# Performance work log

Hardware: AMD Instinct MI355X
Metric: run time of the kernel (lower is better)

## Reference

```python
import jax, jax.numpy as jnp
import numpy as np

B, S, D = 4, 1024, 1024
H, G = 16, 8            # num_heads, num_query_groups
HD = D // H             # head_dim = 64
E, TOPK, ED = 8, 2, 2 * D   # experts, top_k, expert_dim
GH = D // 2             # gate hidden
EPS = 1e-5


def setup_inputs() -> dict:
    key = jax.random.key(0)
    ks = iter(jax.random.split(key, 32))
    rn = lambda shape, s=0.02: jax.random.normal(next(ks), shape, jnp.float32) * s
    return {
        "x": jax.random.normal(next(ks), (B, S, D), jnp.float32),
        # GQA projections (stored [in, out])
        "wq": rn((D, G * HD)), "bq": jnp.zeros((G * HD,), jnp.float32),
        "wk": rn((D, D)), "bk": jnp.zeros((D,), jnp.float32),
        "wv": rn((D, D)), "bv": jnp.zeros((D,), jnp.float32),
        "wo": rn((D, D)), "bo": jnp.zeros((D,), jnp.float32),
        # LayerNorms
        "ln1_g": jnp.ones((D,), jnp.float32), "ln1_b": jnp.zeros((D,), jnp.float32),
        "ln2_g": jnp.ones((D,), jnp.float32), "ln2_b": jnp.zeros((D,), jnp.float32),
        # MoE gate: Linear(D, D//2) -> ReLU -> Linear(D//2, E)
        "gw1": rn((D, GH)), "gb1": jnp.zeros((GH,), jnp.float32),
        "gw2": rn((GH, E)), "gb2": jnp.zeros((E,), jnp.float32),
        # stacked expert FFNs: Linear(D, ED) -> GELU -> Linear(ED, D)
        "ew1": rn((E, D, ED)), "eb1": jnp.zeros((E, ED), jnp.float32),
        "ew2": rn((E, ED, D)), "eb2": jnp.zeros((E, D), jnp.float32),
    }


def _layernorm(x, g, b):
    mu = jnp.mean(x, axis=-1, keepdims=True)
    var = jnp.var(x, axis=-1, keepdims=True)
    return (x - mu) * jax.lax.rsqrt(var + EPS) * g + b


def _block(x, wq, bq, wk, bk, wv, bv, wo, bo, ln1_g, ln1_b, ln2_g, ln2_b,
           gw1, gb1, gw2, gb2, ew1, eb1, ew2, eb2):
    # --- GQA self-attention (dropout is identity in eval) ---
    h = _layernorm(x, ln1_g, ln1_b)
    q = (h @ wq + bq).reshape(B, S, G, HD).transpose(0, 2, 1, 3)   # [B,G,S,hd]
    k = (h @ wk + bk).reshape(B, S, H, HD).transpose(0, 2, 1, 3)   # [B,H,S,hd]
    v = (h @ wv + bv).reshape(B, S, H, HD).transpose(0, 2, 1, 3)
    q = jnp.repeat(q, H // G, axis=1)                              # repeat_interleave -> [B,H,S,hd]
    scores = jnp.einsum("bhqd,bhkd->bhqk", q, k) * (HD ** -0.5)
    attn = jax.nn.softmax(scores, axis=-1)
    ao = jnp.einsum("bhqk,bhkd->bhqd", attn, v)
    ao = ao.transpose(0, 2, 1, 3).reshape(B, S, D) @ wo + bo
    x = x + ao

    # --- MoE FFN ---
    h2 = _layernorm(x, ln2_g, ln2_b).reshape(-1, D)                # [T,D], T=B*S
    gate_logits = jax.nn.relu(h2 @ gw1 + gb1) @ gw2 + gb2          # [T,E]
    gate_w = jax.nn.softmax(gate_logits, axis=-1)
    top_w, top_i = jax.lax.top_k(gate_w, TOPK)                     # [T,k]
    top_w = jax.nn.softmax(top_w, axis=-1)                         # renormalize among top-k
    combine = jnp.sum(jax.nn.one_hot(top_i, E, dtype=h2.dtype) * top_w[..., None], axis=1)  # [T,E]
    hid = jax.nn.gelu(jnp.einsum("td,edh->teh", h2, ew1) + eb1, approximate=False)          # [T,E,ED]
    expert_out = jnp.einsum("teh,ehd->ted", hid, ew2) + eb2        # [T,E,D]
    moe = jnp.einsum("ted,te->td", expert_out, combine).reshape(B, S, D)
    return x + moe


def reference(x, wq, bq, wk, bk, wv, bv, wo, bo, ln1_g, ln1_b, ln2_g, ln2_b,
              gw1, gb1, gw2, gb2, ew1, eb1, ew2, eb2):
    return _block(x, wq, bq, wk, bk, wv, bv, wo, bo, ln1_g, ln1_b, ln2_g, ln2_b,
                  gw1, gb1, gw2, gb2, ew1, eb1, ew2, eb2)
```

## Files before the change

kernel.cpp:

```cpp
#include <hip/hip_runtime.h>

typedef __bf16 bf16x8 __attribute__((ext_vector_type(8)));
typedef float f32x4 __attribute__((ext_vector_type(4)));
typedef unsigned int u32x4 __attribute__((ext_vector_type(4)));
typedef unsigned int u32x2 __attribute__((ext_vector_type(2)));

#define DEV static __device__ __forceinline__

DEV unsigned short f2bf(float f) {
  unsigned int u = __builtin_bit_cast(unsigned int, f);
  u += 0x7fffu + ((u >> 16) & 1u);
  return (unsigned short)(u >> 16);
}
DEV float bf2f(unsigned int hbits) { return __builtin_bit_cast(float, hbits << 16); }

DEV bf16x8 load_bf8(const unsigned short* p) {
  u32x4 u = *(const u32x4*)p;
  return __builtin_bit_cast(bf16x8, u);
}
DEV void unpack8(u32x4 u, float f[8]) {
  f[0] = bf2f(u.x & 0xffffu); f[1] = bf2f(u.x >> 16);
  f[2] = bf2f(u.y & 0xffffu); f[3] = bf2f(u.y >> 16);
  f[4] = bf2f(u.z & 0xffffu); f[5] = bf2f(u.z >> 16);
  f[6] = bf2f(u.w & 0xffffu); f[7] = bf2f(u.w >> 16);
}
DEV void gload_lds16(const void* g, void* l) {
  __builtin_amdgcn_global_load_lds((const __attribute__((address_space(1))) void*)g,
                                   (__attribute__((address_space(3))) void*)l, 16, 0, 0);
}
DEV f32x4 mfma16(bf16x8 a, bf16x8 b, f32x4 c) {
  return __builtin_amdgcn_mfma_f32_16x16x32_bf16(a, b, c, 0, 0, 0);
}

__global__ __launch_bounds__(256) void cm_transpose(
    const float* __restrict__ src, unsigned short* __restrict__ dst,
    int K, int N, long srcStrideE, long dstStrideE) {
  src += (long)blockIdx.z * srcStrideE;
  dst += (long)blockIdx.z * dstStrideE;
  __shared__ float t[32][33];
  const int n0 = blockIdx.x * 32, k0 = blockIdx.y * 32;
  const int tx = threadIdx.x & 31, ty = threadIdx.x >> 5;
#pragma unroll
  for (int j = 0; j < 4; ++j) {
    int k = k0 + ty + j * 8, n = n0 + tx;
    if (k < K && n < N) t[ty + j * 8][tx] = src[(long)k * N + n];
  }
  __syncthreads();
#pragma unroll
  for (int j = 0; j < 4; ++j) {
    int n = n0 + ty + j * 8, k = k0 + tx;
    if (n < N && k < K) dst[(long)n * K + k] = f2bf(t[tx][ty + j * 8]);
  }
}

__global__ __launch_bounds__(256) void cm_transpose_split(
    const float* __restrict__ src, unsigned short* __restrict__ dhi,
    unsigned short* __restrict__ dlo, int K, int N) {
  __shared__ float t[32][33];
  const int n0 = blockIdx.x * 32, k0 = blockIdx.y * 32;
  const int tx = threadIdx.x & 31, ty = threadIdx.x >> 5;
#pragma unroll
  for (int j = 0; j < 4; ++j) {
    int k = k0 + ty + j * 8, n = n0 + tx;
    if (k < K && n < N) t[ty + j * 8][tx] = src[(long)k * N + n];
  }
  __syncthreads();
#pragma unroll
  for (int j = 0; j < 4; ++j) {
    int n = n0 + ty + j * 8, k = k0 + tx;
    if (n < N && k < K) {
      float v = t[tx][ty + j * 8];
      unsigned short hi = f2bf(v);
      dhi[(long)n * K + k] = hi;
      dlo[(long)n * K + k] = f2bf(v - bf2f(hi));
    }
  }
}

template <bool WLO>
__global__ __launch_bounds__(256) void cm_ln(
    const float* __restrict__ x, const float* __restrict__ g, const float* __restrict__ b,
    unsigned short* __restrict__ ob, unsigned short* __restrict__ olo) {
  const int row = blockIdx.x, tid = threadIdx.x;
  const f32x4 v = *(const f32x4*)(x + (long)row * 1024 + tid * 4);
  float s1 = v[0] + v[1] + v[2] + v[3];
  float s2 = v[0] * v[0] + v[1] * v[1] + v[2] * v[2] + v[3] * v[3];
#pragma unroll
  for (int m = 32; m >= 1; m >>= 1) { s1 += __shfl_xor(s1, m); s2 += __shfl_xor(s2, m); }
  __shared__ float r1[4], r2[4];
  if ((tid & 63) == 0) { r1[tid >> 6] = s1; r2[tid >> 6] = s2; }
  __syncthreads();
  s1 = r1[0] + r1[1] + r1[2] + r1[3];
  s2 = r2[0] + r2[1] + r2[2] + r2[3];
  const float mean = s1 * (1.f / 1024.f);
  const float rs = rsqrtf(s2 * (1.f / 1024.f) - mean * mean + 1e-5f);
  const f32x4 gg = *(const f32x4*)(g + tid * 4);
  const f32x4 bb = *(const f32x4*)(b + tid * 4);
  float o[4];
  unsigned short hi[4];
#pragma unroll
  for (int i = 0; i < 4; ++i) {
    o[i] = (v[i] - mean) * rs * gg[i] + bb[i];
    hi[i] = f2bf(o[i]);
  }
  u32x2 pk;
  pk.x = (unsigned)hi[0] | ((unsigned)hi[1] << 16);
  pk.y = (unsigned)hi[2] | ((unsigned)hi[3] << 16);
  *(u32x2*)(ob + (long)row * 1024 + tid * 4) = pk;
  if (WLO) {
    u32x2 pl;
    pl.x = (unsigned)f2bf(o[0] - bf2f(hi[0])) | ((unsigned)f2bf(o[1] - bf2f(hi[1])) << 16);
    pl.y = (unsigned)f2bf(o[2] - bf2f(hi[2])) | ((unsigned)f2bf(o[3] - bf2f(hi[3])) << 16);
    *(u32x2*)(olo + (long)row * 1024 + tid * 4) = pl;
  }
}

enum { EP_BF16 = 0, EP_RELU = 1, EP_GELU = 2, EP_RES_F32 = 3 };

template <int EPI, int MODE>
__global__ __launch_bounds__(256, 2) void cm_gemm_bt(
    const unsigned short* __restrict__ A, int lda,
    const unsigned short* __restrict__ BT, long btStrideE, int ldb,
    const float* __restrict__ bias, int biasStrideE,
    const float* __restrict__ res,
    void* __restrict__ outp, int ldc,
    int M, int K,
    const int* __restrict__ cnt, const int* __restrict__ offs,
    const int* __restrict__ rowidx) {
  int bx, by, z;
  if (MODE == 0) {
    const int gx = gridDim.x, gy = gridDim.y;
    const int nwg = gx * gy;
    int flat = (int)blockIdx.x + gx * (int)blockIdx.y;
    const int q = nwg >> 3, r = nwg & 7, xcd = flat & 7, idx = flat >> 3;
    flat = (xcd < r ? xcd * (q + 1) : r * (q + 1) + (xcd - r) * q) + idx;
    bx = flat % gx; by = flat / gx; z = 0;
  } else {
    bx = blockIdx.x; by = blockIdx.y; z = blockIdx.z;
  }

  int valid = M, rowbase = 0;
  const unsigned short* Bp = BT;
  const float* biasp = bias;
  if (MODE > 0) {
    valid = cnt[z];
    if (by * 128 >= valid) return;
    rowbase = offs[z];
    Bp += (long)z * btStrideE;
    biasp += (long)z * biasStrideE;
  }
  const int tid = threadIdx.x;
  const int brow = by * 128, bcol = bx * 128;
  const int wid = tid >> 6, lane = tid & 63;
  const int wr = wid >> 1, wc = wid & 1;

  const int srow = tid >> 3, sc = tid & 7;
  const int scg = ((sc ^ (srow & 7)) << 3);
  const int ldst = srow * 64 + sc * 8;

  __shared__ __align__(16) unsigned short As[128 * 64];
  __shared__ __align__(16) unsigned short Bs[128 * 64];

  long asrc[4], bsrc[4];
#pragma unroll
  for (int i = 0; i < 4; ++i) {
    int m = brow + srow + i * 32;
    if (MODE == 0) {
      asrc[i] = (long)m * lda;
    } else {
      int p = m < valid ? m : valid - 1;
      if (MODE == 1) asrc[i] = (long)rowidx[z * 4096 + p] * lda;
      else           asrc[i] = (long)(rowbase + p) * lda;
    }
    bsrc[i] = (long)(bcol + srow + i * 32) * ldb;
  }

  f32x4 acc[4][4] = {};

  for (int k0 = 0; k0 < K; k0 += 64) {
#pragma unroll
    for (int i = 0; i < 4; ++i) {
      gload_lds16(A + asrc[i] + k0 + scg, &As[ldst + i * 2048]);
      gload_lds16(Bp + bsrc[i] + k0 + scg, &Bs[ldst + i * 2048]);
    }
    __syncthreads();
#pragma unroll
    for (int ks = 0; ks < 2; ++ks) {
      bf16x8 af[4], bfr[4];
#pragma unroll
      for (int m = 0; m < 4; ++m) {
        const int r = wr * 64 + m * 16 + (lane & 15);
        af[m] = load_bf8(&As[r * 64 + (((ks * 4 + (lane >> 4)) ^ (lane & 7)) << 3)]);
      }
#pragma unroll
      for (int n = 0; n < 4; ++n) {
        const int r = wc * 64 + n * 16 + (lane & 15);
        bfr[n] = load_bf8(&Bs[r * 64 + (((ks * 4 + (lane >> 4)) ^ (lane & 7)) << 3)]);
      }
#pragma unroll
      for (int m = 0; m < 4; ++m)
#pragma unroll
        for (int n = 0; n < 4; ++n)
          acc[m][n] = mfma16(af[m], bfr[n], acc[m][n]);
    }
    __syncthreads();
  }

#pragma unroll
  for (int m = 0; m < 4; ++m) {
#pragma unroll
    for (int rr = 0; rr < 4; ++rr) {
      const int lrow = brow + wr * 64 + m * 16 + (lane >> 4) * 4 + rr;
      if (MODE > 0 && lrow >= valid) continue;
      const long orow = (long)(rowbase + lrow);
#pragma unroll
      for (int n = 0; n < 4; ++n) {
        const int gcol = bcol + wc * 64 + n * 16 + (lane & 15);
        float vv = acc[m][n][rr] + biasp[gcol];
        if constexpr (EPI == EP_RELU) vv = fmaxf(vv, 0.f);
        if constexpr (EPI == EP_GELU) vv = 0.5f * vv * (1.f + erff(vv * 0.70710678f));
        if constexpr (EPI == EP_RES_F32)
          ((float*)outp)[orow * ldc + gcol] = vv + res[orow * ldc + gcol];
        else
          ((unsigned short*)outp)[orow * ldc + gcol] = f2bf(vv);
      }
    }
  }
}

__global__ __launch_bounds__(256, 2) void cm_gemm_gate(
    const unsigned short* __restrict__ Ah, const unsigned short* __restrict__ Al,
    const unsigned short* __restrict__ Bh, const unsigned short* __restrict__ Bl,
    const float* __restrict__ bias, float* __restrict__ C) {
  const int tid = threadIdx.x;
  const int brow = blockIdx.y * 128, bcol = blockIdx.x * 128;
  const int wid = tid >> 6, lane = tid & 63;
  const int wr = wid >> 1, wc = wid & 1;
  const int srow0 = tid >> 2, scol = (tid & 3) * 8;

  __shared__ __align__(16) unsigned short Ash[128 * 32], Asl[128 * 32];
  __shared__ __align__(16) unsigned short Bsh[128 * 32], Bsl[128 * 32];

  f32x4 acc[4][4] = {};

  for (int k0 = 0; k0 < 1024; k0 += 32) {
#pragma unroll
    for (int i = 0; i < 2; ++i) {
      const long ar = (long)(brow + srow0 + i * 64) * 1024 + k0 + scol;
      const long br = (long)(bcol + srow0 + i * 64) * 1024 + k0 + scol;
      const int lo = (srow0 + i * 64) * 32 + scol;
      gload_lds16(Ah + ar, &Ash[lo]);
      gload_lds16(Al + ar, &Asl[lo]);
      gload_lds16(Bh + br, &Bsh[lo]);
      gload_lds16(Bl + br, &Bsl[lo]);
    }
    __syncthreads();
    bf16x8 ah[4], al[4], bh[4], bl[4];
#pragma unroll
    for (int m = 0; m < 4; ++m) {
      const int ro = (wr * 64 + m * 16 + (lane & 15)) * 32 + (lane >> 4) * 8;
      ah[m] = load_bf8(&Ash[ro]); al[m] = load_bf8(&Asl[ro]);
    }
#pragma unroll
    for (int n = 0; n < 4; ++n) {
      const int ro = (wc * 64 + n * 16 + (lane & 15)) * 32 + (lane >> 4) * 8;
      bh[n] = load_bf8(&Bsh[ro]); bl[n] = load_bf8(&Bsl[ro]);
    }
#pragma unroll
    for (int m = 0; m < 4; ++m)
#pragma unroll
      for (int n = 0; n < 4; ++n) {
        acc[m][n] = mfma16(al[m], bh[n], acc[m][n]);
        acc[m][n] = mfma16(ah[m], bl[n], acc[m][n]);
        acc[m][n] = mfma16(ah[m], bh[n], acc[m][n]);
      }
    __syncthreads();
  }

#pragma unroll
  for (int m = 0; m < 4; ++m)
#pragma unroll
    for (int rr = 0; rr < 4; ++rr) {
      const long orow = brow + wr * 64 + m * 16 + (lane >> 4) * 4 + rr;
#pragma unroll
      for (int n = 0; n < 4; ++n) {
        const int gcol = bcol + wc * 64 + n * 16 + (lane & 15);
        C[orow * 512 + gcol] = fmaxf(acc[m][n][rr] + bias[gcol], 0.f);
      }
    }
}

__global__ __launch_bounds__(256) void cm_vtrans(
    const unsigned short* __restrict__ qkv, unsigned short* __restrict__ Vt) {
  const int stile = blockIdx.x, bh = blockIdx.y;
  const int b = bh >> 4, h = bh & 15;
  const int tid = threadIdx.x;
  __shared__ __align__(16) unsigned short t[64][72];
  const int d0 = (tid & 7) * 8, sl = tid >> 3;
#pragma unroll
  for (int i = 0; i < 2; ++i) {
    const int s = sl + i * 32;
    *(u32x4*)&t[s][d0] =
        *(const u32x4*)(qkv + (long)(b * 1024 + stile * 64 + s) * 2560 + 1536 + h * 64 + d0);
  }
  __syncthreads();
  const int s0 = (tid & 7) * 8, dl = tid >> 3;
#pragma unroll
  for (int i = 0; i < 2; ++i) {
    const int d = dl + i * 32;
    unsigned short vals[8];
#pragma unroll
    for (int j = 0; j < 8; ++j) vals[j] = t[s0 + j][d];
    u32x4 u;
    u.x = vals[0] | ((unsigned)vals[1] << 16);
    u.y = vals[2] | ((unsigned)vals[3] << 16);
    u.z = vals[4] | ((unsigned)vals[5] << 16);
    u.w = vals[6] | ((unsigned)vals[7] << 16);
    *(u32x4*)(Vt + (long)(bh * 64 + d) * 1024 + stile * 64 + s0) = u;
  }
}

__global__ __launch_bounds__(256, 2) void cm_attn(
    const unsigned short* __restrict__ qkv,
    const unsigned short* __restrict__ Vt,
    unsigned short* __restrict__ ao) {
  const int qt = blockIdx.x, bh = blockIdx.y;
  const int b = bh >> 4, h = bh & 15, g = h >> 1;
  const int tid = threadIdx.x, wid = tid >> 6, lane = tid & 63;
  const int q0 = qt * 32;

  __shared__ __align__(16) unsigned short sc[32][1032];
  __shared__ float rowrcp[32];

  bf16x8 bq[2][2];
#pragma unroll
  for (int nf = 0; nf < 2; ++nf)
#pragma unroll
    for (int ks = 0; ks < 2; ++ks)
      bq[nf][ks] = load_bf8(qkv + (long)(b * 1024 + q0 + nf * 16 + (lane & 15)) * 2560 +
                            g * 64 + ks * 32 + (lane >> 4) * 8);

#pragma unroll 1
  for (int c = 0; c < 4; ++c) {
    const int kb = wid * 256 + c * 64;
    f32x4 acc[4][2] = {};
#pragma unroll
    for (int ks = 0; ks < 2; ++ks) {
      bf16x8 ak[4];
#pragma unroll
      for (int mf = 0; mf < 4; ++mf)
        ak[mf] = load_bf8(qkv + (long)(b * 1024 + kb + mf * 16 + (lane & 15)) * 2560 +
                          512 + h * 64 + ks * 32 + (lane >> 4) * 8);
#pragma unroll
      for (int mf = 0; mf < 4; ++mf)
#pragma unroll
        for (int nf = 0; nf < 2; ++nf)
          acc[mf][nf] = mfma16(ak[mf], bq[nf][ks], acc[mf][nf]);
    }
#pragma unroll
    for (int mf = 0; mf < 4; ++mf)
#pragma unroll
      for (int nf = 0; nf < 2; ++nf) {
        const int q = nf * 16 + (lane & 15);
        const int key = kb + mf * 16 + (lane >> 4) * 4;
        u32x2 pk;
        pk.x = (unsigned)f2bf(acc[mf][nf][0] * 0.125f) |
               ((unsigned)f2bf(acc[mf][nf][1] * 0.125f) << 16);
        pk.y = (unsigned)f2bf(acc[mf][nf][2] * 0.125f) |
               ((unsigned)f2bf(acc[mf][nf][3] * 0.125f) << 16);
        *(u32x2*)&sc[q][key] = pk;
      }
  }
  __syncthreads();

  {
    const int row = tid >> 3, seg = tid & 7;
    float mx = -1e30f;
#pragma unroll
    for (int i = 0; i < 16; ++i) {
      float f[8];
      unpack8(*(const u32x4*)&sc[row][i * 64 + seg * 8], f);
#pragma unroll
      for (int j = 0; j < 8; ++j) mx = fmaxf(mx, f[j]);
    }
#pragma unroll
    for (int m = 4; m >= 1; m >>= 1) mx = fmaxf(mx, __shfl_xor(mx, m));
    float sum = 0.f;
#pragma unroll 1
    for (int i = 0; i < 16; ++i) {
      float f[8];
      unpack8(*(const u32x4*)&sc[row][i * 64 + seg * 8], f);
      float e[8];
#pragma unroll
      for (int j = 0; j < 8; ++j) { e[j] = __expf(f[j] - mx); sum += e[j]; }
      u32x4 o;
      o.x = (unsigned)f2bf(e[0]) | ((unsigned)f2bf(e[1]) << 16);
      o.y = (unsigned)f2bf(e[2]) | ((unsigned)f2bf(e[3]) << 16);
      o.z = (unsigned)f2bf(e[4]) | ((unsigned)f2bf(e[5]) << 16);
      o.w = (unsigned)f2bf(e[6]) | ((unsigned)f2bf(e[7]) << 16);
      *(u32x4*)&sc[row][i * 64 + seg * 8] = o;
    }
#pragma unroll
    for (int m = 4; m >= 1; m >>= 1) sum += __shfl_xor(sum, m);
    if (seg == 0) rowrcp[row] = 1.f / sum;
  }
  __syncthreads();

  {
    f32x4 acc[2] = {};
    const unsigned short* vtb = Vt + (long)bh * 64 * 1024;
#pragma unroll 4
    for (int k0 = 0; k0 < 1024; k0 += 32) {
      const bf16x8 bv =
          load_bf8(vtb + (long)(wid * 16 + (lane & 15)) * 1024 + k0 + (lane >> 4) * 8);
#pragma unroll
      for (int m = 0; m < 2; ++m) {
        const bf16x8 ap = load_bf8(&sc[m * 16 + (lane & 15)][k0 + (lane >> 4) * 8]);
        acc[m] = mfma16(ap, bv, acc[m]);
      }
    }
#pragma unroll
    for (int m = 0; m < 2; ++m)
#pragma unroll
      for (int rr = 0; rr < 4; ++rr) {
        const int q = m * 16 + (lane >> 4) * 4 + rr;
        const int d = wid * 16 + (lane & 15);
        ao[(long)(b * 1024 + q0 + q) * 1024 + h * 64 + d] = f2bf(acc[m][rr] * rowrcp[q]);
      }
  }
}

__global__ __launch_bounds__(64) void cm_route_pick(
    const float* __restrict__ g1f, const float* __restrict__ gw2, const float* __restrict__ gb2,
    int* __restrict__ pick, int* __restrict__ slot_e, float* __restrict__ rwt) {
  const int t = blockIdx.x, lane = threadIdx.x;
  f32x4 a0 = *(const f32x4*)(g1f + (long)t * 512 + lane * 8);
  f32x4 a1 = *(const f32x4*)(g1f + (long)t * 512 + lane * 8 + 4);
  float logit[8];
#pragma unroll
  for (int e = 0; e < 8; ++e) {
    float s = 0.f;
#pragma unroll
    for (int j = 0; j < 4; ++j) {
      s += a0[j] * gw2[(lane * 8 + j) * 8 + e];
      s += a1[j] * gw2[(lane * 8 + 4 + j) * 8 + e];
    }
#pragma unroll
    for (int m = 32; m >= 1; m >>= 1) s += __shfl_xor(s, m);
    logit[e] = s + gb2[e];
  }
  float mx = logit[0];
#pragma unroll
  for (int e = 1; e < 8; ++e) mx = fmaxf(mx, logit[e]);
  float p[8], sum = 0.f;
#pragma unroll
  for (int e = 0; e < 8; ++e) { p[e] = __expf(logit[e] - mx); sum += p[e]; }
  const float rs = 1.f / sum;
#pragma unroll
  for (int e = 0; e < 8; ++e) p[e] *= rs;
  int i0 = 0;
#pragma unroll
  for (int e = 1; e < 8; ++e) if (p[e] > p[i0]) i0 = e;
  int i1 = (i0 == 0) ? 1 : 0;
#pragma unroll
  for (int e = 0; e < 8; ++e) if (e != i0 && p[e] > p[i1]) i1 = e;
  const float w0 = 1.f / (1.f + __expf(p[i1] - p[i0]));
  if (lane == 0) {
    pick[t] = i0 | (i1 << 8);
    slot_e[t * 2] = i0; slot_e[t * 2 + 1] = i1;
    rwt[t * 2] = w0;    rwt[t * 2 + 1] = 1.f - w0;
  }
}

__global__ __launch_bounds__(256) void cm_route_place(
    const int* __restrict__ pick, int* __restrict__ cnt,
    int* __restrict__ etok, int* __restrict__ slot_p) {
  const int t = blockIdx.x * 256 + threadIdx.x;
  const int lane = threadIdx.x & 63;
  const int pk = pick[t];
  const int p0 = pk & 15, p1 = (pk >> 8) & 15;
  const unsigned long long lt = ((unsigned long long)1 << lane) - 1;
  int my_r0 = 0, my_c0p1 = 0, my_r1 = 0, tot = 0;
#pragma unroll
  for (int e = 0; e < 8; ++e) {
    const unsigned long long m0 = __ballot(p0 == e);
    const unsigned long long m1 = __ballot(p1 == e);
    if (p0 == e) my_r0 = __popcll(m0 & lt);
    if (p1 == e) { my_c0p1 = __popcll(m0); my_r1 = __popcll(m1 & lt); }
    if (lane == e) tot = __popcll(m0) + __popcll(m1);
  }
  int base = 0;
  if (lane < 8 && tot > 0) base = atomicAdd(&cnt[lane], tot);
  const int b0 = __shfl(base, p0);
  const int b1 = __shfl(base, p1);
  const int pos0 = b0 + my_r0;
  const int pos1 = b1 + my_c0p1 + my_r1;
  etok[p0 * 4096 + pos0] = t;
  etok[p1 * 4096 + pos1] = t;
  slot_p[t * 2] = pos0;
  slot_p[t * 2 + 1] = pos1;
}

__global__ void cm_offs(const int* __restrict__ cnt, int* __restrict__ offs) {
  if (threadIdx.x == 0) {
    int s = 0;
#pragma unroll
    for (int e = 0; e < 8; ++e) { offs[e] = s; s += cnt[e]; }
  }
}

__global__ __launch_bounds__(256) void cm_combine(
    const float* __restrict__ x2, const unsigned short* __restrict__ eo,
    const int* __restrict__ slot_e, const int* __restrict__ slot_p,
    const float* __restrict__ rwt, const int* __restrict__ offs,
    float* __restrict__ outp) {
  const int t = blockIdx.x, tid = threadIdx.x;
  const long r0 = (long)(offs[slot_e[t * 2]] + slot_p[t * 2]);
  const long r1 = (long)(offs[slot_e[t * 2 + 1]] + slot_p[t * 2 + 1]);
  const float w0 = rwt[t * 2], w1 = rwt[t * 2 + 1];
  const f32x4 xv = *(const f32x4*)(x2 + (long)t * 1024 + tid * 4);
  u32x2 u0 = *(const u32x2*)(eo + r0 * 1024 + tid * 4);
  u32x2 u1 = *(const u32x2*)(eo + r1 * 1024 + tid * 4);
  f32x4 o;
  o[0] = xv[0] + w0 * bf2f(u0.x & 0xffffu) + w1 * bf2f(u1.x & 0xffffu);
  o[1] = xv[1] + w0 * bf2f(u0.x >> 16) + w1 * bf2f(u1.x >> 16);
  o[2] = xv[2] + w0 * bf2f(u0.y & 0xffffu) + w1 * bf2f(u1.y & 0xffffu);
  o[3] = xv[3] + w0 * bf2f(u0.y >> 16) + w1 * bf2f(u1.y >> 16);
  *(f32x4*)(outp + (long)t * 1024 + tid * 4) = o;
}

extern "C" void kernel_launch(void* const* d_in, const int* in_sizes, int n_in,
                              void* d_out, int out_size, void* d_ws, size_t ws_size,
                              hipStream_t stream) {
  if (n_in < 21) return;
  const float* x    = (const float*)d_in[0];
  const float* wq   = (const float*)d_in[1];
  const float* bq   = (const float*)d_in[2];
  const float* wk   = (const float*)d_in[3];
  const float* bk   = (const float*)d_in[4];
  const float* wv   = (const float*)d_in[5];
  const float* bv   = (const float*)d_in[6];
  const float* wo   = (const float*)d_in[7];
  const float* bo   = (const float*)d_in[8];
  const float* ln1g = (const float*)d_in[9];
  const float* ln1b = (const float*)d_in[10];
  const float* ln2g = (const float*)d_in[11];
  const float* ln2b = (const float*)d_in[12];
  const float* gw1  = (const float*)d_in[13];
  const float* gb1  = (const float*)d_in[14];
  const float* gw2  = (const float*)d_in[15];
  const float* gb2  = (const float*)d_in[16];
  const float* ew1  = (const float*)d_in[17];
  const float* eb1  = (const float*)d_in[18];
  const float* ew2  = (const float*)d_in[19];
  const float* eb2  = (const float*)d_in[20];
  float* outp = (float*)d_out;

  char* ws = (char*)d_ws;
  size_t off = 0;
  auto carve = [&](size_t bytes) -> char* {
    char* p = ws + off;
    off += (bytes + 255) & ~(size_t)255;
    return p;
  };
  unsigned short* wqkvT = (unsigned short*)carve(2560l * 1024 * 2);
  unsigned short* woT   = (unsigned short*)carve(1024l * 1024 * 2);
  unsigned short* gw1hT = (unsigned short*)carve(512l * 1024 * 2);
  unsigned short* gw1lT = (unsigned short*)carve(512l * 1024 * 2);
  unsigned short* ew1T  = (unsigned short*)carve(8l * 2048 * 1024 * 2);
  unsigned short* ew2T  = (unsigned short*)carve(8l * 1024 * 2048 * 2);
  float* bqkv           = (float*)carve(2560 * 4);
  unsigned short* hbuf  = (unsigned short*)carve(4096l * 1024 * 2);
  unsigned short* qkvl  = (unsigned short*)carve(4096l * 2560 * 2);
  unsigned short* Vt    = (unsigned short*)carve(4096l * 1024 * 2);
  unsigned short* ao    = (unsigned short*)carve(4096l * 1024 * 2);
  unsigned short* h2    = (unsigned short*)carve(4096l * 1024 * 2);
  unsigned short* h2lo  = (unsigned short*)carve(4096l * 1024 * 2);
  int* cnt              = (int*)carve(8 * 4);
  int* offs             = (int*)carve(8 * 4);
  int* etok             = (int*)carve(8l * 4096 * 4);
  int* slot_e           = (int*)carve(8192 * 4);
  int* slot_p           = (int*)carve(8192 * 4);
  float* rwt            = (float*)carve(8192 * 4);
  int* pick             = (int*)carve(4096 * 4);
  unsigned short* hid   = (unsigned short*)carve(8192l * 2048 * 2);
  unsigned short* eo    = (unsigned short*)carve(8192l * 1024 * 2);
  if (off > ws_size) return;
  float* x2 = outp;
  float* g1f = (float*)Vt;

  (void)hipMemsetAsync(cnt, 0, 8 * 4, stream);
  (void)hipMemcpyAsync(bqkv, (const void*)bq, 512 * 4, hipMemcpyDeviceToDevice, stream);
  (void)hipMemcpyAsync(bqkv + 512, (const void*)bk, 1024 * 4, hipMemcpyDeviceToDevice, stream);
  (void)hipMemcpyAsync(bqkv + 1536, (const void*)bv, 1024 * 4, hipMemcpyDeviceToDevice, stream);

  cm_transpose<<<dim3(16, 32, 1), 256, 0, stream>>>(wq, wqkvT, 1024, 512, 0l, 0l);
  cm_transpose<<<dim3(32, 32, 1), 256, 0, stream>>>(wk, wqkvT + 512l * 1024, 1024, 1024, 0l, 0l);
  cm_transpose<<<dim3(32, 32, 1), 256, 0, stream>>>(wv, wqkvT + 1536l * 1024, 1024, 1024, 0l, 0l);
  cm_transpose<<<dim3(32, 32, 1), 256, 0, stream>>>(wo, woT, 1024, 1024, 0l, 0l);
  cm_transpose_split<<<dim3(16, 32, 1), 256, 0, stream>>>(gw1, gw1hT, gw1lT, 1024, 512);
  cm_transpose<<<dim3(64, 32, 8), 256, 0, stream>>>(ew1, ew1T, 1024, 2048, 1024l * 2048, 2048l * 1024);
  cm_transpose<<<dim3(32, 64, 8), 256, 0, stream>>>(ew2, ew2T, 2048, 1024, 2048l * 1024, 1024l * 2048);

  cm_ln<false><<<4096, 256, 0, stream>>>(x, ln1g, ln1b, hbuf, nullptr);
  cm_gemm_bt<EP_BF16, 0><<<dim3(20, 32, 1), 256, 0, stream>>>(
      hbuf, 1024, wqkvT, 0l, 1024, bqkv, 0, nullptr, qkvl, 2560, 4096, 1024,
      nullptr, nullptr, nullptr);
  cm_vtrans<<<dim3(16, 64, 1), 256, 0, stream>>>(qkvl, Vt);
  cm_attn<<<dim3(32, 64, 1), 256, 0, stream>>>(qkvl, Vt, ao);
  cm_gemm_bt<EP_RES_F32, 0><<<dim3(8, 32, 1), 256, 0, stream>>>(
      ao, 1024, woT, 0l, 1024, bo, 0, x, x2, 1024, 4096, 1024,
      nullptr, nullptr, nullptr);
  cm_ln<true><<<4096, 256, 0, stream>>>(x2, ln2g, ln2b, h2, h2lo);

  cm_gemm_gate<<<dim3(4, 32, 1), 256, 0, stream>>>(h2, h2lo, gw1hT, gw1lT, gb1, g1f);
  cm_route_pick<<<4096, 64, 0, stream>>>(g1f, gw2, gb2, pick, slot_e, rwt);
  cm_route_place<<<16, 256, 0, stream>>>(pick, cnt, etok, slot_p);
  cm_offs<<<1, 64, 0, stream>>>(cnt, offs);

  cm_gemm_bt<EP_GELU, 1><<<dim3(16, 32, 8), 256, 0, stream>>>(
      h2, 1024, ew1T, 2048l * 1024, 1024, eb1, 2048, nullptr, hid, 2048, 4096, 1024,
      cnt, offs, etok);
  cm_gemm_bt<EP_BF16, 2><<<dim3(8, 32, 8), 256, 0, stream>>>(
      hid, 2048, ew2T, 1024l * 2048, 2048, eb2, 1024, nullptr, eo, 1024, 4096, 2048,
      cnt, offs, nullptr);
  cm_combine<<<4096, 256, 0, stream>>>(x2, eo, slot_e, slot_p, rwt, offs, outp);
}
```

Measured before the change: 449.6 us.

## Shrink attention query tile, fuse exp into score epilogue, swizzle block order

```diff
diff --git a/kernel.cpp b/kernel.cpp
--- a/kernel.cpp
+++ b/kernel.cpp
@@ -13,6 +13,11 @@
   return (unsigned short)(u >> 16);
 }
 DEV float bf2f(unsigned int hbits) { return __builtin_bit_cast(float, hbits << 16); }
+DEV unsigned pack2bf(float a, float b) {
+  unsigned short x = __builtin_bit_cast(unsigned short, (__bf16)a);
+  unsigned short y = __builtin_bit_cast(unsigned short, (__bf16)b);
+  return (unsigned)x | ((unsigned)y << 16);
+}
 
 DEV bf16x8 load_bf8(const unsigned short* p) {
   u32x4 u = *(const u32x4*)p;
@@ -320,30 +325,30 @@
   }
 }
 
-__global__ __launch_bounds__(256, 2) void cm_attn(
+__global__ __launch_bounds__(256, 4) void cm_attn(
     const unsigned short* __restrict__ qkv,
     const unsigned short* __restrict__ Vt,
     unsigned short* __restrict__ ao) {
-  const int qt = blockIdx.x, bh = blockIdx.y;
+  int flat = (int)blockIdx.x + (int)gridDim.x * (int)blockIdx.y;
+  flat = (flat & 7) * 512 + (flat >> 3);
+  const int qt = flat & 63, bh = flat >> 6;
   const int b = bh >> 4, h = bh & 15, g = h >> 1;
   const int tid = threadIdx.x, wid = tid >> 6, lane = tid & 63;
-  const int q0 = qt * 32;
-
-  __shared__ __align__(16) unsigned short sc[32][1032];
-  __shared__ float rowrcp[32];
-
-  bf16x8 bq[2][2];
-#pragma unroll
-  for (int nf = 0; nf < 2; ++nf)
-#pragma unroll
-    for (int ks = 0; ks < 2; ++ks)
-      bq[nf][ks] = load_bf8(qkv + (long)(b * 1024 + q0 + nf * 16 + (lane & 15)) * 2560 +
-                            g * 64 + ks * 32 + (lane >> 4) * 8);
+  const int q0 = qt * 16;
+
+  __shared__ __align__(16) unsigned short sc[16][1032];
+  __shared__ float rowrcp[16];
+
+  bf16x8 bq[2];
+#pragma unroll
+  for (int ks = 0; ks < 2; ++ks)
+    bq[ks] = load_bf8(qkv + (long)(b * 1024 + q0 + (lane & 15)) * 2560 +
+                      g * 64 + ks * 32 + (lane >> 4) * 8);
 
 #pragma unroll 1
   for (int c = 0; c < 4; ++c) {
     const int kb = wid * 256 + c * 64;
-    f32x4 acc[4][2] = {};
+    f32x4 acc[4] = {};
 #pragma unroll
     for (int ks = 0; ks < 2; ++ks) {
       bf16x8 ak[4];
@@ -353,80 +358,52 @@
                           512 + h * 64 + ks * 32 + (lane >> 4) * 8);
 #pragma unroll
       for (int mf = 0; mf < 4; ++mf)
-#pragma unroll
-        for (int nf = 0; nf < 2; ++nf)
-          acc[mf][nf] = mfma16(ak[mf], bq[nf][ks], acc[mf][nf]);
-    }
-#pragma unroll
-    for (int mf = 0; mf < 4; ++mf)
-#pragma unroll
-      for (int nf = 0; nf < 2; ++nf) {
-        const int q = nf * 16 + (lane & 15);
-        const int key = kb + mf * 16 + (lane >> 4) * 4;
-        u32x2 pk;
-        pk.x = (unsigned)f2bf(acc[mf][nf][0] * 0.125f) |
-               ((unsigned)f2bf(acc[mf][nf][1] * 0.125f) << 16);
-        pk.y = (unsigned)f2bf(acc[mf][nf][2] * 0.125f) |
-               ((unsigned)f2bf(acc[mf][nf][3] * 0.125f) << 16);
-        *(u32x2*)&sc[q][key] = pk;
-      }
+        acc[mf] = mfma16(ak[mf], bq[ks], acc[mf]);
+    }
+#pragma unroll
+    for (int mf = 0; mf < 4; ++mf) {
+      const int q = lane & 15;
+      const int key = kb + mf * 16 + (lane >> 4) * 4;
+      u32x2 pk;
+      pk.x = pack2bf(__expf(acc[mf][0] * 0.125f), __expf(acc[mf][1] * 0.125f));
+      pk.y = pack2bf(__expf(acc[mf][2] * 0.125f), __expf(acc[mf][3] * 0.125f));
+      *(u32x2*)&sc[q][key] = pk;
+    }
   }
   __syncthreads();
 
   {
-    const int row = tid >> 3, seg = tid & 7;
-    float mx = -1e30f;
-#pragma unroll
-    for (int i = 0; i < 16; ++i) {
+    const int row = tid >> 4, seg = tid & 15;
+    float sum = 0.f;
+#pragma unroll
+    for (int i = 0; i < 8; ++i) {
       float f[8];
-      unpack8(*(const u32x4*)&sc[row][i * 64 + seg * 8], f);
-#pragma unroll
-      for (int j = 0; j < 8; ++j) mx = fmaxf(mx, f[j]);
-    }
-#pragma unroll
-    for (int m = 4; m >= 1; m >>= 1) mx = fmaxf(mx, __shfl_xor(mx, m));
-    float sum = 0.f;
-#pragma unroll 1
-    for (int i = 0; i < 16; ++i) {
-      float f[8];
-      unpack8(*(const u32x4*)&sc[row][i * 64 + seg * 8], f);
-      float e[8];
-#pragma unroll
-      for (int j = 0; j < 8; ++j) { e[j] = __expf(f[j] - mx); sum += e[j]; }
-      u32x4 o;
-      o.x = (unsigned)f2bf(e[0]) | ((unsigned)f2bf(e[1]) << 16);
-      o.y = (unsigned)f2bf(e[2]) | ((unsigned)f2bf(e[3]) << 16);
-      o.z = (unsigned)f2bf(e[4]) | ((unsigned)f2bf(e[5]) << 16);
-      o.w = (unsigned)f2bf(e[6]) | ((unsigned)f2bf(e[7]) << 16);
-      *(u32x4*)&sc[row][i * 64 + seg * 8] = o;
-    }
-#pragma unroll
-    for (int m = 4; m >= 1; m >>= 1) sum += __shfl_xor(sum, m);
+      unpack8(*(const u32x4*)&sc[row][i * 128 + seg * 8], f);
+#pragma unroll
+      for (int j = 0; j < 8; ++j) sum += f[j];
+    }
+#pragma unroll
+    for (int m = 8; m >= 1; m >>= 1) sum += __shfl_xor(sum, m);
     if (seg == 0) rowrcp[row] = 1.f / sum;
   }
   __syncthreads();
 
   {
-    f32x4 acc[2] = {};
+    f32x4 acc = {};
     const unsigned short* vtb = Vt + (long)bh * 64 * 1024;
 #pragma unroll 4
     for (int k0 = 0; k0 < 1024; k0 += 32) {
       const bf16x8 bv =
           load_bf8(vtb + (long)(wid * 16 + (lane & 15)) * 1024 + k0 + (lane >> 4) * 8);
-#pragma unroll
-      for (int m = 0; m < 2; ++m) {
-        const bf16x8 ap = load_bf8(&sc[m * 16 + (lane & 15)][k0 + (lane >> 4) * 8]);
-        acc[m] = mfma16(ap, bv, acc[m]);
-      }
-    }
-#pragma unroll
-    for (int m = 0; m < 2; ++m)
-#pragma unroll
-      for (int rr = 0; rr < 4; ++rr) {
-        const int q = m * 16 + (lane >> 4) * 4 + rr;
-        const int d = wid * 16 + (lane & 15);
-        ao[(long)(b * 1024 + q0 + q) * 1024 + h * 64 + d] = f2bf(acc[m][rr] * rowrcp[q]);
-      }
+      const bf16x8 ap = load_bf8(&sc[lane & 15][k0 + (lane >> 4) * 8]);
+      acc = mfma16(ap, bv, acc);
+    }
+#pragma unroll
+    for (int rr = 0; rr < 4; ++rr) {
+      const int q = (lane >> 4) * 4 + rr;
+      const int d = wid * 16 + (lane & 15);
+      ao[(long)(b * 1024 + q0 + q) * 1024 + h * 64 + d] = f2bf(acc[rr] * rowrcp[q]);
+    }
   }
 }
 
@@ -607,7 +584,7 @@
       hbuf, 1024, wqkvT, 0l, 1024, bqkv, 0, nullptr, qkvl, 2560, 4096, 1024,
       nullptr, nullptr, nullptr);
   cm_vtrans<<<dim3(16, 64, 1), 256, 0, stream>>>(qkvl, Vt);
-  cm_attn<<<dim3(32, 64, 1), 256, 0, stream>>>(qkvl, Vt, ao);
+  cm_attn<<<dim3(64, 64, 1), 256, 0, stream>>>(qkvl, Vt, ao);
   cm_gemm_bt<EP_RES_F32, 0><<<dim3(8, 32, 1), 256, 0, stream>>>(
       ao, 1024, woT, 0l, 1024, bo, 0, x, x2, 1024, 4096, 1024,
       nullptr, nullptr, nullptr);
```

After: 487.5 us. 8.4% more time.
